# Kernel optimization log

Hardware: AMD Instinct MI355X
Metric: run time of the kernel (lower is better)

The kernel has to match this reference:

```python
import jax, jax.numpy as jnp
import numpy as np

N, C, H, W = 8, 128, 128, 128   # batch, emb channels, spatial
O, M, K, L = 81, 1, 3, 3        # classes, num_modes, neg_num_modes, neg MPC layers
SIGMA, BETA, NEG_SCOPE = 0.5, 0.3, 2.0
EPS = 1e-12


def _l2norm(v, axis):
    # matches F.normalize: v / max(||v||, eps)
    n = jnp.sqrt(jnp.sum(v * v, axis=axis, keepdims=True))
    return v / jnp.maximum(n, EPS)


def setup_inputs() -> dict:
    key = jax.random.key(0)
    k0, k1, k2 = jax.random.split(key, 3)
    return {
        "x": jax.random.normal(k0, (N, C, H, W), jnp.float32),
        "rep_fc_w": jax.random.normal(k1, (O * M * C,), jnp.float32) * 0.01,
        "rep_fc_b": jnp.zeros((O * M * C,), jnp.float32),
        "neg_w": jax.random.normal(k2, (K, L, C, C), jnp.float32) * 0.01,
        "neg_b": jnp.zeros((K, L, C), jnp.float32),
    }


def reference(x, rep_fc_w, rep_fc_b, neg_w, neg_b):
    # emb_module = identity; L2-normalize embeddings over channel dim
    e = _l2norm(x, axis=1)                      # (N,C,H,W)
    ehw = e.transpose(0, 2, 3, 1)               # (N,H,W,C)

    # reps = rep_fc(1.0) -> weight + bias (Linear(1, O*M*C) applied to scalar 1)
    reps = (rep_fc_w + rep_fc_b).reshape(O, M, C)
    reps = _l2norm(reps, axis=2)                # (O,1,C) unit rows

    # negative reps: K independent 3-layer MLPs (ReLU between layers)
    r = reps[:, 0, :]                           # (O,C)
    neg_list = []
    for k in range(K):
        h = r
        for l in range(L):
            h = h @ neg_w[k, l].T + neg_b[k, l]
            if l < L - 1:
                h = jax.nn.relu(h)
        neg_list.append(h)
    reps_neg = jnp.stack(neg_list, axis=1)      # (O,K,C)
    reps_neg = _l2norm(reps_neg, axis=2)

    # Both sides unit-norm -> ||e - r||^2 = 2 - 2<e,r>; compute via GEMM
    dot = jnp.einsum('nhwc,omc->nomhw', ehw, reps)        # (N,O,M,H,W)
    distances = jnp.sqrt(jax.nn.relu(2.0 - 2.0 * dot))
    dot_n = jnp.einsum('nhwc,okc->nokhw', ehw, reps_neg)  # (N,O,K,H,W)
    distances_neg = jnp.sqrt(jax.nn.relu(2.0 - 2.0 * dot_n))

    inv = 1.0 / (2.0 * SIGMA ** 2)
    probs_neg = jnp.exp(-distances_neg ** 2 * inv)
    cls_score_neg = probs_neg.max(axis=2)                 # (N,O,H,W)

    probs_ori = jnp.exp(-distances ** 2 * inv).max(axis=2)  # (N,O,H,W)

    min_neg = distances_neg.min(axis=2, keepdims=True)    # (N,O,1,H,W)
    probs = jnp.exp(-(distances + BETA * jax.nn.relu(NEG_SCOPE - min_neg)) ** 2 * inv)

    # cls_norm = True: normalize summed probs over classes
    probs_sumj = probs.sum(axis=2)                        # (N,O,H,W)
    cls_score = probs_sumj / probs_sumj.sum(axis=1, keepdims=True)

    return (cls_score, cls_score_neg, distances, distances_neg, probs_ori)
```

## Files before the change

### kernel.cpp

```cpp
#include <hip/hip_runtime.h>

#define HW 16384

typedef __attribute__((ext_vector_type(8))) short bf16x8;
typedef __attribute__((ext_vector_type(4))) float f32x4;

static constexpr size_t OFF0 = 0;
static constexpr size_t OFF1 = 10616832;
static constexpr size_t OFF2 = 21233664;
static constexpr size_t OFF3 = 31850496;
static constexpr size_t OFF4 = 63700992;

static __device__ __forceinline__ unsigned short f2bf(float f) {
  unsigned int u = __float_as_uint(f);
  u += 0x7fffu + ((u >> 16) & 1u);
  return (unsigned short)(u >> 16);
}

static __device__ __forceinline__ void frag_write(unsigned short* wsA, int R, int j,
                                                  unsigned short v) {
  const int mt = R >> 4;
  const int ks = j >> 5;
  const int hi = (j >> 3) & 3;
  const int jj = j & 7;
  const int lane = hi * 16 + (R & 15);
  wsA[((size_t)((mt * 4 + ks) * 64 + lane)) * 8 + jj] = v;
}

__global__ __launch_bounds__(128) void prep_all(const float* __restrict__ rw,
                                                const float* __restrict__ rb,
                                                const float* __restrict__ nw,
                                                const float* __restrict__ nb,
                                                unsigned short* __restrict__ wsA) {
  const int b = blockIdx.x;
  const int k = b / 81, o = b % 81;
  const int j = threadIdx.x;
  __shared__ __align__(16) float hrow[128];
  __shared__ float red[2];

  float v = rw[o * 128 + j] + rb[o * 128 + j];
  float sq = v * v;
#pragma unroll
  for (int m = 1; m < 64; m <<= 1) sq += __shfl_xor(sq, m, 64);
  if ((j & 63) == 0) red[j >> 6] = sq;
  __syncthreads();
  const float r = v / fmaxf(sqrtf(red[0] + red[1]), 1e-12f);
  __syncthreads();
  hrow[j] = r;
  __syncthreads();

  float acc = 0.f;
#pragma unroll
  for (int l = 0; l < 3; ++l) {
    const float4* Wr = (const float4*)(nw + (((size_t)(k * 3 + l)) * 128 + j) * 128);
    const float4* H  = (const float4*)hrow;
    float4 a = {0.f, 0.f, 0.f, 0.f};
#pragma unroll
    for (int q = 0; q < 32; ++q) {
      float4 wv = Wr[q]; float4 hv = H[q];
      a.x = fmaf(wv.x, hv.x, a.x); a.y = fmaf(wv.y, hv.y, a.y);
      a.z = fmaf(wv.z, hv.z, a.z); a.w = fmaf(wv.w, hv.w, a.w);
    }
    acc = (a.x + a.y) + (a.z + a.w) + nb[(k * 3 + l) * 128 + j];
    if (l < 2) acc = fmaxf(acc, 0.f);
    __syncthreads();
    if (l < 2) hrow[j] = acc;
    __syncthreads();
  }

  float sq2 = acc * acc;
#pragma unroll
  for (int m = 1; m < 64; m <<= 1) sq2 += __shfl_xor(sq2, m, 64);
  if ((j & 63) == 0) red[j >> 6] = sq2;
  __syncthreads();
  const float accn = acc / fmaxf(sqrtf(red[0] + red[1]), 1e-12f);

  frag_write(wsA, o * 4 + k + 1, j, f2bf(accn));
  if (k == 0) frag_write(wsA, o * 4, j, f2bf(r));
  if (b == 0) {
#pragma unroll
    for (int R = 324; R < 336; ++R) frag_write(wsA, R, j, (unsigned short)0);
  }
}

__global__ __launch_bounds__(256) void main_kernel(const float* __restrict__ x,
                                                   const bf16x8* __restrict__ wsA,
                                                   float* __restrict__ out) {
  __shared__ __align__(16) char eLds[32768];
  __shared__ float ss[8][128];
  __shared__ float invn[128];

  const int b = blockIdx.x;
  const int n = b >> 7;
  const int p0 = (b & 127) << 7;
  const int t = threadIdx.x;
  const float* xb = x + ((size_t)n * 128) * HW + p0;

  {
    const int pq = (t & 31) * 4;
    const int cg = t >> 5;
    const int swz = (t & 7) << 4;
    float a0 = 0.f, a1 = 0.f, a2 = 0.f, a3 = 0.f;
#pragma unroll
    for (int i = 0; i < 4; ++i) {
      const int c0 = i * 32 + cg * 4;
      float4 v0 = *(const float4*)(xb + (size_t)(c0 + 0) * HW + pq);
      float4 v1 = *(const float4*)(xb + (size_t)(c0 + 1) * HW + pq);
      float4 v2 = *(const float4*)(xb + (size_t)(c0 + 2) * HW + pq);
      float4 v3 = *(const float4*)(xb + (size_t)(c0 + 3) * HW + pq);
      a0 = fmaf(v0.x, v0.x, fmaf(v1.x, v1.x, fmaf(v2.x, v2.x, fmaf(v3.x, v3.x, a0))));
      a1 = fmaf(v0.y, v0.y, fmaf(v1.y, v1.y, fmaf(v2.y, v2.y, fmaf(v3.y, v3.y, a1))));
      a2 = fmaf(v0.z, v0.z, fmaf(v1.z, v1.z, fmaf(v2.z, v2.z, fmaf(v3.z, v3.z, a2))));
      a3 = fmaf(v0.w, v0.w, fmaf(v1.w, v1.w, fmaf(v2.w, v2.w, fmaf(v3.w, v3.w, a3))));
      uint2 w;
      w.x = (unsigned)f2bf(v0.x) | ((unsigned)f2bf(v1.x) << 16);
      w.y = (unsigned)f2bf(v2.x) | ((unsigned)f2bf(v3.x) << 16);
      *(uint2*)(eLds + (((pq + 0) * 256 + c0 * 2) ^ swz)) = w;
      w.x = (unsigned)f2bf(v0.y) | ((unsigned)f2bf(v1.y) << 16);
      w.y = (unsigned)f2bf(v2.y) | ((unsigned)f2bf(v3.y) << 16);
      *(uint2*)(eLds + (((pq + 1) * 256 + c0 * 2) ^ swz)) = w;
      w.x = (unsigned)f2bf(v0.z) | ((unsigned)f2bf(v1.z) << 16);
      w.y = (unsigned)f2bf(v2.z) | ((unsigned)f2bf(v3.z) << 16);
      *(uint2*)(eLds + (((pq + 2) * 256 + c0 * 2) ^ swz)) = w;
      w.x = (unsigned)f2bf(v0.w) | ((unsigned)f2bf(v1.w) << 16);
      w.y = (unsigned)f2bf(v2.w) | ((unsigned)f2bf(v3.w) << 16);
      *(uint2*)(eLds + (((pq + 3) * 256 + c0 * 2) ^ swz)) = w;
    }
    float4 st = {a0, a1, a2, a3};
    *(float4*)&ss[cg][pq] = st;
  }
  __syncthreads();
  if (t < 128) {
    float s = 0.f;
#pragma unroll
    for (int g = 0; g < 8; ++g) s += ss[g][t];
    invn[t] = 1.f / fmaxf(sqrtf(s), 1e-12f);
  }
  __syncthreads();

  const int lane = t & 63;
  const int wv = t >> 6;
  const int og = lane >> 4;

  bf16x8 bfrag[2][4];
  float ivp[2];
#pragma unroll
  for (int u = 0; u < 2; ++u) {
    const int p = (wv * 2 + u) * 16 + (lane & 15);
    const int swzr = ((p >> 2) & 7) << 4;
#pragma unroll
    for (int ks = 0; ks < 4; ++ks) {
      const int addr = (p * 256 + ks * 64 + (lane >> 4) * 16) ^ swzr;
      bfrag[u][ks] = *(const bf16x8*)(eLds + addr);
    }
    ivp[u] = invn[p];
  }

  float probs_arr[42];

#pragma unroll
  for (int mt = 0; mt < 21; ++mt) {
    bf16x8 afr[4];
#pragma unroll
    for (int ks = 0; ks < 4; ++ks) afr[ks] = wsA[(mt * 4 + ks) * 64 + lane];
    f32x4 c0 = {0.f, 0.f, 0.f, 0.f}, c1 = {0.f, 0.f, 0.f, 0.f};
#pragma unroll
    for (int ks = 0; ks < 4; ++ks) {
      c0 = __builtin_amdgcn_mfma_f32_16x16x32_bf16(afr[ks], bfrag[0][ks], c0, 0, 0, 0);
      c1 = __builtin_amdgcn_mfma_f32_16x16x32_bf16(afr[ks], bfrag[1][ks], c1, 0, 0, 0);
    }
    const int o = mt * 4 + og;
    const bool valid = (o < 81);
#pragma unroll
    for (int u = 0; u < 2; ++u) {
      const f32x4 c = u ? c1 : c0;
      const float iv = ivp[u];
      float q0 = fmaxf(2.f - 2.f * (c[0] * iv), 0.f);
      float d0 = sqrtf(q0);
      float d1 = sqrtf(fmaxf(2.f - 2.f * (c[1] * iv), 0.f));
      float d2 = sqrtf(fmaxf(2.f - 2.f * (c[2] * iv), 0.f));
      float d3 = sqrtf(fmaxf(2.f - 2.f * (c[3] * iv), 0.f));
      float dmin = fminf(d1, fminf(d2, d3));
      float pneg = __expf(-2.f * dmin * dmin);
      float pori = __expf(-2.f * q0);
      float tt = d0 + 0.3f * fmaxf(2.f - dmin, 0.f);
      float pr = __expf(-2.f * tt * tt);
      probs_arr[mt * 2 + u] = valid ? pr : 0.f;
      if (valid) {
        const int pimg = p0 + (wv * 2 + u) * 16 + (lane & 15);
        const size_t base = ((size_t)(n * 81 + o)) * HW + pimg;
        out[OFF2 + base] = d0;
        out[OFF4 + base] = pori;
        out[OFF1 + base] = pneg;
        const size_t b3 = ((size_t)((n * 81 + o) * 3)) * HW + pimg;
        out[OFF3 + b3] = d1;
        out[OFF3 + b3 + HW] = d2;
        out[OFF3 + b3 + 2 * HW] = d3;
      }
    }
  }

#pragma unroll
  for (int u = 0; u < 2; ++u) {
    float s = 0.f;
#pragma unroll
    for (int mt = 0; mt < 21; ++mt) s += probs_arr[mt * 2 + u];
    s += __shfl_xor(s, 16, 64);
    s += __shfl_xor(s, 32, 64);
    const float is = 1.f / s;
    const int pimg = p0 + (wv * 2 + u) * 16 + (lane & 15);
#pragma unroll
    for (int mt = 0; mt < 21; ++mt) {
      const int o = mt * 4 + og;
      if (o < 81) {
        const size_t base = ((size_t)(n * 81 + o)) * HW + pimg;
        out[OFF0 + base] = probs_arr[mt * 2 + u] * is;
      }
    }
  }
}

extern "C" void kernel_launch(void* const* d_in, const int* in_sizes, int n_in,
                              void* d_out, int out_size, void* d_ws, size_t ws_size,
                              hipStream_t stream) {
  const float* x  = (const float*)d_in[0];
  const float* rw = (const float*)d_in[1];
  const float* rb = (const float*)d_in[2];
  const float* nw = (const float*)d_in[3];
  const float* nb = (const float*)d_in[4];
  float* out = (float*)d_out;
  unsigned short* wsA_us = (unsigned short*)d_ws;
  const bf16x8* wsA = (const bf16x8*)d_ws;

  hipLaunchKernelGGL(prep_all, dim3(243), dim3(128), 0, stream, rw, rb, nw, nb, wsA_us);
  hipLaunchKernelGGL(main_kernel, dim3(1024), dim3(256), 0, stream, x, wsA, out);
}
```

Baseline: 97.93 us.

## Stage outputs through LDS to emit vectorized nontemporal float4 stores

Each wave now writes its per-lane scalar results (distances, neg probs, ori probs, normalized scores) into a private region of the reused LDS buffer. It then reads them back as float4 and issues 16-byte nontemporal global stores, replacing scattered 4-byte stores. The aim is better store coalescing and less cache pollution on a write-bound kernel. It also computes pneg from the squared minimum instead of squaring a sqrt, and it adds LDS traffic and index arithmetic. Because there is no barrier between the ds writes and reads, correctness relies on same-wave ordering.

```diff
diff --git a/kernel.cpp b/kernel.cpp
--- a/kernel.cpp
+++ b/kernel.cpp
@@ -2,8 +2,8 @@
 
 #define HW 16384
 
-typedef __attribute__((ext_vector_type(8))) short bf16x8;
-typedef __attribute__((ext_vector_type(4))) float f32x4;
+typedef short bf16x8 __attribute__((ext_vector_type(8)));
+typedef float f32x4 __attribute__((ext_vector_type(4)));
 
 static constexpr size_t OFF0 = 0;
 static constexpr size_t OFF1 = 10616832;
@@ -141,12 +141,13 @@
   const int lane = t & 63;
   const int wv = t >> 6;
   const int og = lane >> 4;
+  const int px16 = lane & 15;
 
   bf16x8 bfrag[2][4];
   float ivp[2];
 #pragma unroll
   for (int u = 0; u < 2; ++u) {
-    const int p = (wv * 2 + u) * 16 + (lane & 15);
+    const int p = (wv * 2 + u) * 16 + px16;
     const int swzr = ((p >> 2) & 7) << 4;
 #pragma unroll
     for (int ks = 0; ks < 4; ++ks) {
@@ -155,6 +156,8 @@
     }
     ivp[u] = invn[p];
   }
+
+  float* stg = (float*)(eLds + wv * 8192);
 
   float probs_arr[42];
 
@@ -176,30 +179,46 @@
       const f32x4 c = u ? c1 : c0;
       const float iv = ivp[u];
       float q0 = fmaxf(2.f - 2.f * (c[0] * iv), 0.f);
-      float d0 = sqrtf(q0);
-      float d1 = sqrtf(fmaxf(2.f - 2.f * (c[1] * iv), 0.f));
-      float d2 = sqrtf(fmaxf(2.f - 2.f * (c[2] * iv), 0.f));
-      float d3 = sqrtf(fmaxf(2.f - 2.f * (c[3] * iv), 0.f));
+      float q1 = fmaxf(2.f - 2.f * (c[1] * iv), 0.f);
+      float q2 = fmaxf(2.f - 2.f * (c[2] * iv), 0.f);
+      float q3 = fmaxf(2.f - 2.f * (c[3] * iv), 0.f);
+      float d0 = sqrtf(q0), d1 = sqrtf(q1), d2 = sqrtf(q2), d3 = sqrtf(q3);
+      float qmin = fminf(q1, fminf(q2, q3));
       float dmin = fminf(d1, fminf(d2, d3));
-      float pneg = __expf(-2.f * dmin * dmin);
+      float pneg = __expf(-2.f * qmin);
       float pori = __expf(-2.f * q0);
       float tt = d0 + 0.3f * fmaxf(2.f - dmin, 0.f);
       float pr = __expf(-2.f * tt * tt);
       probs_arr[mt * 2 + u] = valid ? pr : 0.f;
-      if (valid) {
-        const int pimg = p0 + (wv * 2 + u) * 16 + (lane & 15);
-        const size_t base = ((size_t)(n * 81 + o)) * HW + pimg;
-        out[OFF2 + base] = d0;
-        out[OFF4 + base] = pori;
-        out[OFF1 + base] = pneg;
-        const size_t b3 = ((size_t)((n * 81 + o) * 3)) * HW + pimg;
-        out[OFF3 + b3] = d1;
-        out[OFF3 + b3 + HW] = d2;
-        out[OFF3 + b3 + 2 * HW] = d3;
+      float* su = stg + u * 480 + og * 120 + px16;
+      su[0] = d0; su[20] = d1; su[40] = d2; su[60] = d3;
+      su[80] = pneg; su[100] = pori;
+    }
+#pragma unroll
+    for (int pass = 0; pass < 3; ++pass) {
+      const int slot = pass * 64 + lane;
+      const int pair = slot >> 2;
+      const int quad = slot & 3;
+      const int uu = pair >= 24;
+      const int pr6 = pair - 24 * uu;
+      const int ol = (pr6 * 43) >> 8;
+      const int j = pr6 - 6 * ol;
+      const int oo = mt * 4 + ol;
+      f32x4 v = *(const f32x4*)(stg + pair * 20 + quad * 4);
+      if (oo < 81) {
+        const int px = p0 + wv * 32 + uu * 16 + quad * 4;
+        const int idx81 = n * 81 + oo;
+        size_t off;
+        if (j == 0) off = OFF2 + (size_t)idx81 * HW;
+        else if (j < 4) off = OFF3 + ((size_t)(idx81 * 3 + (j - 1))) * HW;
+        else if (j == 4) off = OFF1 + (size_t)idx81 * HW;
+        else off = OFF4 + (size_t)idx81 * HW;
+        __builtin_nontemporal_store(v, (f32x4*)(out + off + px));
       }
     }
   }
 
+  float isv[2];
 #pragma unroll
   for (int u = 0; u < 2; ++u) {
     float s = 0.f;
@@ -207,14 +226,35 @@
     for (int mt = 0; mt < 21; ++mt) s += probs_arr[mt * 2 + u];
     s += __shfl_xor(s, 16, 64);
     s += __shfl_xor(s, 32, 64);
-    const float is = 1.f / s;
-    const int pimg = p0 + (wv * 2 + u) * 16 + (lane & 15);
-#pragma unroll
-    for (int mt = 0; mt < 21; ++mt) {
-      const int o = mt * 4 + og;
-      if (o < 81) {
-        const size_t base = ((size_t)(n * 81 + o)) * HW + pimg;
-        out[OFF0 + base] = probs_arr[mt * 2 + u] * is;
+    isv[u] = 1.f / s;
+  }
+#pragma unroll
+  for (int g = 0; g < 6; ++g) {
+    const int nmt = (g < 5) ? 4 : 1;
+#pragma unroll
+    for (int mtl = 0; mtl < 4; ++mtl) {
+      if (mtl < nmt) {
+        const int mt = g * 4 + mtl;
+#pragma unroll
+        for (int u = 0; u < 2; ++u)
+          stg[u * 320 + (mtl * 4 + og) * 20 + px16] = probs_arr[mt * 2 + u] * isv[u];
+      }
+    }
+#pragma unroll
+    for (int pass = 0; pass < 2; ++pass) {
+      const int slot = pass * 64 + lane;
+      const int pair = slot >> 2;
+      const int quad = slot & 3;
+      const int uu = pair >= 16;
+      const int pp = pair - 16 * uu;
+      const int mtl = pp >> 2;
+      const int ol = pp & 3;
+      const int oo = (g * 4 + mtl) * 4 + ol;
+      f32x4 v = *(const f32x4*)(stg + pair * 20 + quad * 4);
+      if (mtl < nmt && oo < 81) {
+        const int px = p0 + wv * 32 + uu * 16 + quad * 4;
+        const size_t off = OFF0 + (size_t)(n * 81 + oo) * HW;
+        __builtin_nontemporal_store(v, (f32x4*)(out + off + px));
       }
     }
   }
```

After: 98.86 us. No clear change (+1.0%).

## Make each wave self-contained, drop block barriers, use nontemporal stores and fast math

Applied to the files above, without the earlier changes.

Each wave now loads and normalizes its own 32 pixels into a private LDS slice and reduces the channel norms with cross-lane shuffles. This removes the two block-wide __syncthreads and the shared partial-sum table. Output stores become nontemporal to bypass cache pollution on the large write stream, and sqrt, reciprocal and rsqrt use the hardware approximate builtins, with pneg taken from the min of squared distances. Each wave's global loads now cover 32 pixels instead of 128, so the read segments are narrower, and the approximate math slightly changes numerics.

```diff
diff --git a/kernel.cpp b/kernel.cpp
--- a/kernel.cpp
+++ b/kernel.cpp
@@ -2,8 +2,8 @@
 
 #define HW 16384
 
-typedef __attribute__((ext_vector_type(8))) short bf16x8;
-typedef __attribute__((ext_vector_type(4))) float f32x4;
+typedef short bf16x8 __attribute__((ext_vector_type(8)));
+typedef float f32x4 __attribute__((ext_vector_type(4)));
 
 static constexpr size_t OFF0 = 0;
 static constexpr size_t OFF1 = 10616832;
@@ -86,28 +86,33 @@
 __global__ __launch_bounds__(256) void main_kernel(const float* __restrict__ x,
                                                    const bf16x8* __restrict__ wsA,
                                                    float* __restrict__ out) {
-  __shared__ __align__(16) char eLds[32768];
-  __shared__ float ss[8][128];
-  __shared__ float invn[128];
+  __shared__ __align__(16) char lds[4 * 8448];
 
   const int b = blockIdx.x;
   const int n = b >> 7;
   const int p0 = (b & 127) << 7;
   const int t = threadIdx.x;
-  const float* xb = x + ((size_t)n * 128) * HW + p0;
+  const int lane = t & 63;
+  const int wv = t >> 6;
+
+  char* slice = lds + wv * 8448;
+  float* invn = (float*)(slice + 8192);
+  const int P0 = p0 + wv * 32;
+  const float* xw = x + ((size_t)n * 128) * HW + P0;
 
   {
-    const int pq = (t & 31) * 4;
-    const int cg = t >> 5;
-    const int swz = (t & 7) << 4;
+    const int q = lane & 7;
+    const int cb = lane >> 3;
+    const int pq = q * 4;
+    const int swz = q << 4;
     float a0 = 0.f, a1 = 0.f, a2 = 0.f, a3 = 0.f;
 #pragma unroll
     for (int i = 0; i < 4; ++i) {
-      const int c0 = i * 32 + cg * 4;
-      float4 v0 = *(const float4*)(xb + (size_t)(c0 + 0) * HW + pq);
-      float4 v1 = *(const float4*)(xb + (size_t)(c0 + 1) * HW + pq);
-      float4 v2 = *(const float4*)(xb + (size_t)(c0 + 2) * HW + pq);
-      float4 v3 = *(const float4*)(xb + (size_t)(c0 + 3) * HW + pq);
+      const int c0 = i * 32 + cb * 4;
+      float4 v0 = *(const float4*)(xw + (size_t)(c0 + 0) * HW + pq);
+      float4 v1 = *(const float4*)(xw + (size_t)(c0 + 1) * HW + pq);
+      float4 v2 = *(const float4*)(xw + (size_t)(c0 + 2) * HW + pq);
+      float4 v3 = *(const float4*)(xw + (size_t)(c0 + 3) * HW + pq);
       a0 = fmaf(v0.x, v0.x, fmaf(v1.x, v1.x, fmaf(v2.x, v2.x, fmaf(v3.x, v3.x, a0))));
       a1 = fmaf(v0.y, v0.y, fmaf(v1.y, v1.y, fmaf(v2.y, v2.y, fmaf(v3.y, v3.y, a1))));
       a2 = fmaf(v0.z, v0.z, fmaf(v1.z, v1.z, fmaf(v2.z, v2.z, fmaf(v3.z, v3.z, a2))));
@@ -115,43 +120,47 @@
       uint2 w;
       w.x = (unsigned)f2bf(v0.x) | ((unsigned)f2bf(v1.x) << 16);
       w.y = (unsigned)f2bf(v2.x) | ((unsigned)f2bf(v3.x) << 16);
-      *(uint2*)(eLds + (((pq + 0) * 256 + c0 * 2) ^ swz)) = w;
+      *(uint2*)(slice + (((pq + 0) * 256 + c0 * 2) ^ swz)) = w;
       w.x = (unsigned)f2bf(v0.y) | ((unsigned)f2bf(v1.y) << 16);
       w.y = (unsigned)f2bf(v2.y) | ((unsigned)f2bf(v3.y) << 16);
-      *(uint2*)(eLds + (((pq + 1) * 256 + c0 * 2) ^ swz)) = w;
+      *(uint2*)(slice + (((pq + 1) * 256 + c0 * 2) ^ swz)) = w;
       w.x = (unsigned)f2bf(v0.z) | ((unsigned)f2bf(v1.z) << 16);
       w.y = (unsigned)f2bf(v2.z) | ((unsigned)f2bf(v3.z) << 16);
-      *(uint2*)(eLds + (((pq + 2) * 256 + c0 * 2) ^ swz)) = w;
+      *(uint2*)(slice + (((pq + 2) * 256 + c0 * 2) ^ swz)) = w;
       w.x = (unsigned)f2bf(v0.w) | ((unsigned)f2bf(v1.w) << 16);
       w.y = (unsigned)f2bf(v2.w) | ((unsigned)f2bf(v3.w) << 16);
-      *(uint2*)(eLds + (((pq + 3) * 256 + c0 * 2) ^ swz)) = w;
-    }
-    float4 st = {a0, a1, a2, a3};
-    *(float4*)&ss[cg][pq] = st;
-  }
-  __syncthreads();
-  if (t < 128) {
-    float s = 0.f;
-#pragma unroll
-    for (int g = 0; g < 8; ++g) s += ss[g][t];
-    invn[t] = 1.f / fmaxf(sqrtf(s), 1e-12f);
-  }
-  __syncthreads();
-
-  const int lane = t & 63;
-  const int wv = t >> 6;
+      *(uint2*)(slice + (((pq + 3) * 256 + c0 * 2) ^ swz)) = w;
+    }
+#pragma unroll
+    for (int m = 8; m < 64; m <<= 1) {
+      a0 += __shfl_xor(a0, m, 64);
+      a1 += __shfl_xor(a1, m, 64);
+      a2 += __shfl_xor(a2, m, 64);
+      a3 += __shfl_xor(a3, m, 64);
+    }
+    if (lane < 8) {
+      float4 iv;
+      iv.x = __builtin_amdgcn_rsqf(fmaxf(a0, 1e-24f));
+      iv.y = __builtin_amdgcn_rsqf(fmaxf(a1, 1e-24f));
+      iv.z = __builtin_amdgcn_rsqf(fmaxf(a2, 1e-24f));
+      iv.w = __builtin_amdgcn_rsqf(fmaxf(a3, 1e-24f));
+      *(float4*)(invn + pq) = iv;
+    }
+  }
+
   const int og = lane >> 4;
+  const int px16 = lane & 15;
 
   bf16x8 bfrag[2][4];
   float ivp[2];
 #pragma unroll
   for (int u = 0; u < 2; ++u) {
-    const int p = (wv * 2 + u) * 16 + (lane & 15);
+    const int p = u * 16 + px16;
     const int swzr = ((p >> 2) & 7) << 4;
 #pragma unroll
     for (int ks = 0; ks < 4; ++ks) {
       const int addr = (p * 256 + ks * 64 + (lane >> 4) * 16) ^ swzr;
-      bfrag[u][ks] = *(const bf16x8*)(eLds + addr);
+      bfrag[u][ks] = *(const bf16x8*)(slice + addr);
     }
     ivp[u] = invn[p];
   }
@@ -176,26 +185,30 @@
       const f32x4 c = u ? c1 : c0;
       const float iv = ivp[u];
       float q0 = fmaxf(2.f - 2.f * (c[0] * iv), 0.f);
-      float d0 = sqrtf(q0);
-      float d1 = sqrtf(fmaxf(2.f - 2.f * (c[1] * iv), 0.f));
-      float d2 = sqrtf(fmaxf(2.f - 2.f * (c[2] * iv), 0.f));
-      float d3 = sqrtf(fmaxf(2.f - 2.f * (c[3] * iv), 0.f));
+      float q1 = fmaxf(2.f - 2.f * (c[1] * iv), 0.f);
+      float q2 = fmaxf(2.f - 2.f * (c[2] * iv), 0.f);
+      float q3 = fmaxf(2.f - 2.f * (c[3] * iv), 0.f);
+      float d0 = __builtin_amdgcn_sqrtf(q0);
+      float d1 = __builtin_amdgcn_sqrtf(q1);
+      float d2 = __builtin_amdgcn_sqrtf(q2);
+      float d3 = __builtin_amdgcn_sqrtf(q3);
+      float qmin = fminf(q1, fminf(q2, q3));
       float dmin = fminf(d1, fminf(d2, d3));
-      float pneg = __expf(-2.f * dmin * dmin);
+      float pneg = __expf(-2.f * qmin);
       float pori = __expf(-2.f * q0);
       float tt = d0 + 0.3f * fmaxf(2.f - dmin, 0.f);
       float pr = __expf(-2.f * tt * tt);
       probs_arr[mt * 2 + u] = valid ? pr : 0.f;
       if (valid) {
-        const int pimg = p0 + (wv * 2 + u) * 16 + (lane & 15);
+        const int pimg = P0 + u * 16 + px16;
         const size_t base = ((size_t)(n * 81 + o)) * HW + pimg;
-        out[OFF2 + base] = d0;
-        out[OFF4 + base] = pori;
-        out[OFF1 + base] = pneg;
+        __builtin_nontemporal_store(d0, out + OFF2 + base);
+        __builtin_nontemporal_store(pori, out + OFF4 + base);
+        __builtin_nontemporal_store(pneg, out + OFF1 + base);
         const size_t b3 = ((size_t)((n * 81 + o) * 3)) * HW + pimg;
-        out[OFF3 + b3] = d1;
-        out[OFF3 + b3 + HW] = d2;
-        out[OFF3 + b3 + 2 * HW] = d3;
+        __builtin_nontemporal_store(d1, out + OFF3 + b3);
+        __builtin_nontemporal_store(d2, out + OFF3 + b3 + HW);
+        __builtin_nontemporal_store(d3, out + OFF3 + b3 + 2 * HW);
       }
     }
   }
@@ -207,14 +220,14 @@
     for (int mt = 0; mt < 21; ++mt) s += probs_arr[mt * 2 + u];
     s += __shfl_xor(s, 16, 64);
     s += __shfl_xor(s, 32, 64);
-    const float is = 1.f / s;
-    const int pimg = p0 + (wv * 2 + u) * 16 + (lane & 15);
+    const float is = __builtin_amdgcn_rcpf(s);
+    const int pimg = P0 + u * 16 + px16;
 #pragma unroll
     for (int mt = 0; mt < 21; ++mt) {
       const int o = mt * 4 + og;
       if (o < 81) {
         const size_t base = ((size_t)(n * 81 + o)) * HW + pimg;
-        out[OFF0 + base] = probs_arr[mt * 2 + u] * is;
+        __builtin_nontemporal_store(probs_arr[mt * 2 + u] * is, out + OFF0 + base);
       }
     }
   }
```

New measurement: 103.7 us. +5.9%, slower.

## Stage outputs through LDS for coalesced vector nontemporal stores with larger blocks

Applied to the files above, without the earlier changes.

Block size grows from 256 to 512 threads and each block now covers 256 pixels. Per-class results are staged in a padded LDS buffer so they can be written as contiguous float4 nontemporal stores instead of scattered scalar stores. The probs are packed to bf16 in registers to cut register pressure, and rsq/rcp/sqrt intrinsics replace the full-precision calls. The price is about 73KB of LDS per block and two barriers per class tile, which limits occupancy and adds sync overhead, and the bf16-rounded probs lower the precision of cls_score.

```diff
diff --git a/kernel.cpp b/kernel.cpp
--- a/kernel.cpp
+++ b/kernel.cpp
@@ -2,14 +2,16 @@
 
 #define HW 16384
 
-typedef __attribute__((ext_vector_type(8))) short bf16x8;
-typedef __attribute__((ext_vector_type(4))) float f32x4;
+typedef short bf16x8 __attribute__((ext_vector_type(8)));
+typedef float f32x4 __attribute__((ext_vector_type(4)));
 
 static constexpr size_t OFF0 = 0;
 static constexpr size_t OFF1 = 10616832;
 static constexpr size_t OFF2 = 21233664;
 static constexpr size_t OFF3 = 31850496;
 static constexpr size_t OFF4 = 63700992;
+
+#define STG_STRIDE 264
 
 static __device__ __forceinline__ unsigned short f2bf(float f) {
   unsigned int u = __float_as_uint(f);
@@ -83,27 +85,29 @@
   }
 }
 
-__global__ __launch_bounds__(256) void main_kernel(const float* __restrict__ x,
-                                                   const bf16x8* __restrict__ wsA,
-                                                   float* __restrict__ out) {
-  __shared__ __align__(16) char eLds[32768];
-  __shared__ float ss[8][128];
-  __shared__ float invn[128];
+__global__ __launch_bounds__(512, 4) void main_kernel(const float* __restrict__ x,
+                                                      const bf16x8* __restrict__ wsA,
+                                                      float* __restrict__ out) {
+  __shared__ __align__(16) char lds[74752];
+  float* ss   = (float*)(lds + 65536);
+  float* invn = (float*)(lds + 73728);
+  float* stg  = (float*)lds;
 
   const int b = blockIdx.x;
-  const int n = b >> 7;
-  const int p0 = (b & 127) << 7;
+  const int n = b >> 6;
+  const int p0 = (b & 63) << 8;
   const int t = threadIdx.x;
+  const int lane = t & 63;
+  const int w = t >> 6;
   const float* xb = x + ((size_t)n * 128) * HW + p0;
 
   {
-    const int pq = (t & 31) * 4;
-    const int cg = t >> 5;
+    const int pq = (t & 63) * 4;
     const int swz = (t & 7) << 4;
     float a0 = 0.f, a1 = 0.f, a2 = 0.f, a3 = 0.f;
 #pragma unroll
     for (int i = 0; i < 4; ++i) {
-      const int c0 = i * 32 + cg * 4;
+      const int c0 = i * 32 + w * 4;
       float4 v0 = *(const float4*)(xb + (size_t)(c0 + 0) * HW + pq);
       float4 v1 = *(const float4*)(xb + (size_t)(c0 + 1) * HW + pq);
       float4 v2 = *(const float4*)(xb + (size_t)(c0 + 2) * HW + pq);
@@ -112,51 +116,51 @@
       a1 = fmaf(v0.y, v0.y, fmaf(v1.y, v1.y, fmaf(v2.y, v2.y, fmaf(v3.y, v3.y, a1))));
       a2 = fmaf(v0.z, v0.z, fmaf(v1.z, v1.z, fmaf(v2.z, v2.z, fmaf(v3.z, v3.z, a2))));
       a3 = fmaf(v0.w, v0.w, fmaf(v1.w, v1.w, fmaf(v2.w, v2.w, fmaf(v3.w, v3.w, a3))));
-      uint2 w;
-      w.x = (unsigned)f2bf(v0.x) | ((unsigned)f2bf(v1.x) << 16);
-      w.y = (unsigned)f2bf(v2.x) | ((unsigned)f2bf(v3.x) << 16);
-      *(uint2*)(eLds + (((pq + 0) * 256 + c0 * 2) ^ swz)) = w;
-      w.x = (unsigned)f2bf(v0.y) | ((unsigned)f2bf(v1.y) << 16);
-      w.y = (unsigned)f2bf(v2.y) | ((unsigned)f2bf(v3.y) << 16);
-      *(uint2*)(eLds + (((pq + 1) * 256 + c0 * 2) ^ swz)) = w;
-      w.x = (unsigned)f2bf(v0.z) | ((unsigned)f2bf(v1.z) << 16);
-      w.y = (unsigned)f2bf(v2.z) | ((unsigned)f2bf(v3.z) << 16);
-      *(uint2*)(eLds + (((pq + 2) * 256 + c0 * 2) ^ swz)) = w;
-      w.x = (unsigned)f2bf(v0.w) | ((unsigned)f2bf(v1.w) << 16);
-      w.y = (unsigned)f2bf(v2.w) | ((unsigned)f2bf(v3.w) << 16);
-      *(uint2*)(eLds + (((pq + 3) * 256 + c0 * 2) ^ swz)) = w;
+      uint2 wd;
+      wd.x = (unsigned)f2bf(v0.x) | ((unsigned)f2bf(v1.x) << 16);
+      wd.y = (unsigned)f2bf(v2.x) | ((unsigned)f2bf(v3.x) << 16);
+      *(uint2*)(lds + (((pq + 0) * 256 + c0 * 2) ^ swz)) = wd;
+      wd.x = (unsigned)f2bf(v0.y) | ((unsigned)f2bf(v1.y) << 16);
+      wd.y = (unsigned)f2bf(v2.y) | ((unsigned)f2bf(v3.y) << 16);
+      *(uint2*)(lds + (((pq + 1) * 256 + c0 * 2) ^ swz)) = wd;
+      wd.x = (unsigned)f2bf(v0.z) | ((unsigned)f2bf(v1.z) << 16);
+      wd.y = (unsigned)f2bf(v2.z) | ((unsigned)f2bf(v3.z) << 16);
+      *(uint2*)(lds + (((pq + 2) * 256 + c0 * 2) ^ swz)) = wd;
+      wd.x = (unsigned)f2bf(v0.w) | ((unsigned)f2bf(v1.w) << 16);
+      wd.y = (unsigned)f2bf(v2.w) | ((unsigned)f2bf(v3.w) << 16);
+      *(uint2*)(lds + (((pq + 3) * 256 + c0 * 2) ^ swz)) = wd;
     }
     float4 st = {a0, a1, a2, a3};
-    *(float4*)&ss[cg][pq] = st;
-  }
-  __syncthreads();
-  if (t < 128) {
+    *(float4*)&ss[w * 256 + pq] = st;
+  }
+  __syncthreads();
+  if (t < 256) {
     float s = 0.f;
 #pragma unroll
-    for (int g = 0; g < 8; ++g) s += ss[g][t];
-    invn[t] = 1.f / fmaxf(sqrtf(s), 1e-12f);
-  }
-  __syncthreads();
-
-  const int lane = t & 63;
-  const int wv = t >> 6;
+    for (int g = 0; g < 8; ++g) s += ss[g * 256 + t];
+    invn[t] = __builtin_amdgcn_rsqf(fmaxf(s, 1e-24f));
+  }
+  __syncthreads();
+
   const int og = lane >> 4;
+  const int px16 = lane & 15;
 
   bf16x8 bfrag[2][4];
   float ivp[2];
 #pragma unroll
   for (int u = 0; u < 2; ++u) {
-    const int p = (wv * 2 + u) * 16 + (lane & 15);
+    const int p = w * 32 + u * 16 + px16;
     const int swzr = ((p >> 2) & 7) << 4;
 #pragma unroll
     for (int ks = 0; ks < 4; ++ks) {
       const int addr = (p * 256 + ks * 64 + (lane >> 4) * 16) ^ swzr;
-      bfrag[u][ks] = *(const bf16x8*)(eLds + addr);
+      bfrag[u][ks] = *(const bf16x8*)(lds + addr);
     }
     ivp[u] = invn[p];
   }
-
-  float probs_arr[42];
+  __syncthreads();
+
+  unsigned probs_pk[21];
 
 #pragma unroll
   for (int mt = 0; mt < 21; ++mt) {
@@ -171,52 +175,96 @@
     }
     const int o = mt * 4 + og;
     const bool valid = (o < 81);
+    float pru[2];
 #pragma unroll
     for (int u = 0; u < 2; ++u) {
       const f32x4 c = u ? c1 : c0;
       const float iv = ivp[u];
       float q0 = fmaxf(2.f - 2.f * (c[0] * iv), 0.f);
-      float d0 = sqrtf(q0);
-      float d1 = sqrtf(fmaxf(2.f - 2.f * (c[1] * iv), 0.f));
-      float d2 = sqrtf(fmaxf(2.f - 2.f * (c[2] * iv), 0.f));
-      float d3 = sqrtf(fmaxf(2.f - 2.f * (c[3] * iv), 0.f));
+      float q1 = fmaxf(2.f - 2.f * (c[1] * iv), 0.f);
+      float q2 = fmaxf(2.f - 2.f * (c[2] * iv), 0.f);
+      float q3 = fmaxf(2.f - 2.f * (c[3] * iv), 0.f);
+      float d0 = __builtin_amdgcn_sqrtf(q0);
+      float d1 = __builtin_amdgcn_sqrtf(q1);
+      float d2 = __builtin_amdgcn_sqrtf(q2);
+      float d3 = __builtin_amdgcn_sqrtf(q3);
+      float qmin = fminf(q1, fminf(q2, q3));
       float dmin = fminf(d1, fminf(d2, d3));
-      float pneg = __expf(-2.f * dmin * dmin);
+      float pneg = __expf(-2.f * qmin);
       float pori = __expf(-2.f * q0);
       float tt = d0 + 0.3f * fmaxf(2.f - dmin, 0.f);
       float pr = __expf(-2.f * tt * tt);
-      probs_arr[mt * 2 + u] = valid ? pr : 0.f;
-      if (valid) {
-        const int pimg = p0 + (wv * 2 + u) * 16 + (lane & 15);
-        const size_t base = ((size_t)(n * 81 + o)) * HW + pimg;
-        out[OFF2 + base] = d0;
-        out[OFF4 + base] = pori;
-        out[OFF1 + base] = pneg;
-        const size_t b3 = ((size_t)((n * 81 + o) * 3)) * HW + pimg;
-        out[OFF3 + b3] = d1;
-        out[OFF3 + b3 + HW] = d2;
-        out[OFF3 + b3 + 2 * HW] = d3;
+      pru[u] = valid ? pr : 0.f;
+      float* su = stg + og * 6 * STG_STRIDE + w * 32 + u * 16 + px16;
+      su[0] = d0;
+      su[1 * STG_STRIDE] = d1;
+      su[2 * STG_STRIDE] = d2;
+      su[3 * STG_STRIDE] = d3;
+      su[4 * STG_STRIDE] = pneg;
+      su[5 * STG_STRIDE] = pori;
+    }
+    probs_pk[mt] = ((unsigned)f2bf(pru[1]) << 16) | (unsigned)f2bf(pru[0]);
+    __syncthreads();
+#pragma unroll
+    for (int r = 0; r < 3; ++r) {
+      const int m = w * 3 + r;
+      const int ogm = m / 6, jv = m % 6;
+      const int oo = mt * 4 + ogm;
+      f32x4 v = *(const f32x4*)(stg + m * STG_STRIDE + lane * 4);
+      if (oo < 81) {
+        const size_t idx81 = (size_t)(n * 81 + oo);
+        size_t off;
+        if (jv == 0) off = OFF2 + idx81 * HW;
+        else if (jv <= 3) off = OFF3 + (idx81 * 3 + (jv - 1)) * HW;
+        else if (jv == 4) off = OFF1 + idx81 * HW;
+        else off = OFF4 + idx81 * HW;
+        __builtin_nontemporal_store(v, (f32x4*)(out + off + p0 + lane * 4));
       }
     }
-  }
-
-#pragma unroll
-  for (int u = 0; u < 2; ++u) {
-    float s = 0.f;
-#pragma unroll
-    for (int mt = 0; mt < 21; ++mt) s += probs_arr[mt * 2 + u];
-    s += __shfl_xor(s, 16, 64);
-    s += __shfl_xor(s, 32, 64);
-    const float is = 1.f / s;
-    const int pimg = p0 + (wv * 2 + u) * 16 + (lane & 15);
-#pragma unroll
-    for (int mt = 0; mt < 21; ++mt) {
-      const int o = mt * 4 + og;
-      if (o < 81) {
-        const size_t base = ((size_t)(n * 81 + o)) * HW + pimg;
-        out[OFF0 + base] = probs_arr[mt * 2 + u] * is;
+    __syncthreads();
+  }
+
+  float s0 = 0.f, s1 = 0.f;
+#pragma unroll
+  for (int mt = 0; mt < 21; ++mt) {
+    s0 += __uint_as_float(probs_pk[mt] << 16);
+    s1 += __uint_as_float(probs_pk[mt] & 0xffff0000u);
+  }
+  s0 += __shfl_xor(s0, 16, 64); s0 += __shfl_xor(s0, 32, 64);
+  s1 += __shfl_xor(s1, 16, 64); s1 += __shfl_xor(s1, 32, 64);
+  const float is0 = __builtin_amdgcn_rcpf(s0);
+  const float is1 = __builtin_amdgcn_rcpf(s1);
+
+#pragma unroll
+  for (int g = 0; g < 4; ++g) {
+    const int nj = (g < 3) ? 6 : 3;
+#pragma unroll
+    for (int j = 0; j < 6; ++j) {
+      if (j < nj) {
+        const int mt = g * 6 + j;
+        const float v0 = __uint_as_float(probs_pk[mt] << 16) * is0;
+        const float v1 = __uint_as_float(probs_pk[mt] & 0xffff0000u) * is1;
+        float* su = stg + (j * 4 + og) * STG_STRIDE + w * 32 + px16;
+        su[0] = v0;
+        su[16] = v1;
       }
     }
+    __syncthreads();
+    const int nrows = nj * 4;
+#pragma unroll
+    for (int r = 0; r < 3; ++r) {
+      const int m = w * 3 + r;
+      if (m < nrows) {
+        const int j = m >> 2, ogm = m & 3;
+        const int oo = (g * 6 + j) * 4 + ogm;
+        f32x4 v = *(const f32x4*)(stg + m * STG_STRIDE + lane * 4);
+        if (oo < 81) {
+          __builtin_nontemporal_store(
+              v, (f32x4*)(out + OFF0 + (size_t)(n * 81 + oo) * HW + p0 + lane * 4));
+        }
+      }
+    }
+    __syncthreads();
   }
 }
 
@@ -233,5 +281,5 @@
   const bf16x8* wsA = (const bf16x8*)d_ws;
 
   hipLaunchKernelGGL(prep_all, dim3(243), dim3(128), 0, stream, rw, rb, nw, nb, wsA_us);
-  hipLaunchKernelGGL(main_kernel, dim3(1024), dim3(256), 0, stream, x, wsA, out);
-}
+  hipLaunchKernelGGL(main_kernel, dim3(512), dim3(512), 0, stream, x, wsA, out);
+}
```

Measured after the change: 104.1 us. 6.3% more time.
